# Kernel tuning notes

Measured on AMD Instinct MI355X. Metric: run time of the kernel, lower is better.

## Reference

```python
import jax, jax.numpy as jnp
import numpy as np

N = 100000
E = 1600000
IN_C, HID_C, OUT_C = 128, 128, 64


def setup_inputs() -> dict:
    key = jax.random.key(0)
    ks = jax.random.split(key, 8)
    x = jax.random.normal(ks[0], (N, IN_C), dtype=jnp.float32)
    edge_index = jax.random.randint(ks[1], (2, E), 0, N, dtype=jnp.int64)
    # Glorot-ish init for the 3 GCNConv linear weights + zero biases (PyG default)
    def glorot(k, fan_in, fan_out):
        s = jnp.sqrt(6.0 / (fan_in + fan_out))
        return jax.random.uniform(k, (fan_in, fan_out), jnp.float32, -s, s)
    return {
        "x": x,
        "edge_index": edge_index,
        "W1": glorot(ks[2], IN_C, HID_C), "b1": jnp.zeros((HID_C,), jnp.float32),
        "W2": glorot(ks[3], HID_C, HID_C), "b2": jnp.zeros((HID_C,), jnp.float32),
        "W3": glorot(ks[4], HID_C, OUT_C), "b3": jnp.zeros((OUT_C,), jnp.float32),
    }


def _gcn_norm(edge_index, num_nodes):
    # add self loops, compute D^-1/2 (A+I) D^-1/2 edge coefficients (PyG gcn_norm)
    loop = jnp.arange(num_nodes, dtype=edge_index.dtype)
    src = jnp.concatenate([edge_index[0], loop])  # [E+N]
    dst = jnp.concatenate([edge_index[1], loop])
    w = jnp.ones_like(src, dtype=jnp.float32)
    deg = jax.ops.segment_sum(w, dst, num_segments=num_nodes)
    dinv = jnp.where(deg > 0, jax.lax.rsqrt(deg), 0.0)
    norm = dinv[src] * dinv[dst]  # [E+N]
    return src, dst, norm


def _gcn_layer(x, src, dst, norm, W, b, num_nodes):
    h = x @ W                                   # [N, out]
    msg = h[src] * norm[:, None]                # gather + scale, [E+N, out]
    agg = jax.ops.segment_sum(msg, dst, num_segments=num_nodes)  # scatter-add
    return agg + b


def reference(x, edge_index, W1, b1, W2, b2, W3, b3):
    src, dst, norm = _gcn_norm(edge_index, N)
    h = jax.nn.relu(_gcn_layer(x, src, dst, norm, W1, b1, N))
    h = jax.nn.relu(_gcn_layer(h, src, dst, norm, W2, b2, N))
    h = _gcn_layer(h, src, dst, norm, W3, b3, N)
    return jax.nn.log_softmax(h, axis=-1)  # [N, OUT_C]
```

## Files before the change

kernel.cpp:

```cpp
#include <hip/hip_runtime.h>
#include <hip/hip_bf16.h>


constexpr int N_NODES = 100000;
constexpr int E_EDGES = 1600000;
constexpr int NB = (N_NODES + 127) / 128;
constexpr int BCAP = 2560;
constexpr int CHUNK = 4096;
constexpr int NCHUNK = (E_EDGES + CHUNK - 1) / CHUNK;

typedef short bf16x8 __attribute__((ext_vector_type(8)));
typedef float f32x4 __attribute__((ext_vector_type(4)));

__device__ __forceinline__ unsigned short f2bf(float f) {
    unsigned u = __float_as_uint(f);
    unsigned r = (u + 0x7fff + ((u >> 16) & 1)) >> 16;
    return (unsigned short)r;
}
__device__ __forceinline__ float bf_lo(unsigned u) { return __uint_as_float(u << 16); }
__device__ __forceinline__ float bf_hi(unsigned u) { return __uint_as_float(u & 0xffff0000u); }
__device__ __forceinline__ unsigned pack2bf(float lo, float hi) {
    return (unsigned)f2bf(lo) | ((unsigned)f2bf(hi) << 16);
}

__device__ __forceinline__ int get_idx(const void* ei, int use64, long long pos) {
    if (use64) return (int)((const long long*)ei)[pos];
    return ((const int*)ei)[pos];
}

__global__ void prep_wt_kernel(const float* __restrict__ W1, const float* __restrict__ W2,
                               const float* __restrict__ W3,
                               unsigned short* __restrict__ WT1,
                               unsigned short* __restrict__ WT2,
                               unsigned short* __restrict__ WT3,
                               const int* __restrict__ ei32, int* __restrict__ flag,
                               int* __restrict__ cursorPad) {
    const int b = blockIdx.x;
    if (b == 3) {
        for (int i = threadIdx.x; i < NB * 16; i += blockDim.x) cursorPad[i] = 0;
        if (threadIdx.x == 0) {
            int ok64 = 1;
#pragma unroll
            for (int i = 1; i < 64; i += 2) ok64 &= (ei32[i] == 0);
            *flag = ok64;
        }
        return;
    }
    const float* W = (b == 0) ? W1 : (b == 1) ? W2 : W3;
    unsigned short* WT = (b == 0) ? WT1 : (b == 1) ? WT2 : WT3;
    const int COUT = (b == 2) ? 64 : 128;
    for (int i = threadIdx.x; i < COUT * 128; i += blockDim.x) {
        int c = i >> 7;
        int k = i & 127;
        WT[c * 128 + k] = f2bf(W[k * COUT + c]);
    }
}

__global__ __launch_bounds__(256) void scatter_direct(
    const void* __restrict__ ei, const int* __restrict__ flag,
    int* __restrict__ cursorPad, unsigned* __restrict__ pairs) {
    __shared__ int h[NB];
    __shared__ int base[NB];
    __shared__ unsigned dstb[CHUNK];
    const int t = threadIdx.x;
    const int use64 = *flag;
    const int e0 = blockIdx.x * CHUNK;
    const int e1 = min(E_EDGES, e0 + CHUNK);

    for (int i = t; i < NB; i += 256) h[i] = 0;
    __syncthreads();
    for (int e = e0 + t; e < e1; e += 256) {
        unsigned d = (unsigned)get_idx(ei, use64, (long long)E_EDGES + e);
        dstb[e - e0] = d;
        atomicAdd(&h[d >> 7], 1);
    }
    __syncthreads();
    for (int i = t; i < NB; i += 256) {
        int c = h[i];
        if (c) base[i] = atomicAdd(&cursorPad[i * 16], c);
        h[i] = 0;
    }
    __syncthreads();
    for (int e = e0 + t; e < e1; e += 256) {
        unsigned s = (unsigned)get_idx(ei, use64, e);
        unsigned d = dstb[e - e0];
        int b = d >> 7;
        int r = base[b] + atomicAdd(&h[b], 1);
        if (r < BCAP) pairs[(unsigned)b * BCAP + r] = (s << 7) | (d & 127u);
    }
}

__global__ __launch_bounds__(256) void fine_sort_kernel(
    const unsigned* __restrict__ pairs, const int* __restrict__ cursorPad,
    int* __restrict__ csr, int* __restrict__ rowptr, int* __restrict__ deg,
    float* __restrict__ dinv) {
    __shared__ int h[128];
    __shared__ int rp[128];
    __shared__ int sc[128];
    const int t = threadIdx.x;
    const int b = blockIdx.x;
    const int base = b * BCAP;
    const int cnt = min(cursorPad[b * 16], BCAP);

    if (t < 128) h[t] = 0;
    __syncthreads();
    for (int i = t; i < cnt; i += 256) {
        unsigned p = pairs[base + i];
        atomicAdd(&h[p & 127u], 1);
    }
    __syncthreads();
    int v = (t < 128) ? h[t] : 0;
    if (t < 128) sc[t] = v;
    __syncthreads();
    int incl = v;
    for (int off = 1; off < 128; off <<= 1) {
        int add = (t >= off && t < 128) ? sc[t - off] : 0;
        __syncthreads();
        if (t < 128) {
            incl += add;
            sc[t] = incl;
        }
        __syncthreads();
    }
    if (t < 128) {
        rp[t] = incl - v;
        int node = b * 128 + t;
        if (node < N_NODES) {
            rowptr[node] = base + incl - v;
            deg[node] = v;
            dinv[node] = rsqrtf((float)(v + 1));
        }
        h[t] = 0;
    }
    __syncthreads();
    for (int i = t; i < cnt; i += 256) {
        unsigned p = pairs[base + i];
        int l = (int)(p & 127u);
        int r = atomicAdd(&h[l], 1);
        csr[base + rp[l] + r] = (int)(p >> 7);
    }
}

template <int COUT>
__global__ __launch_bounds__(256) void gemm_mfma_f32(const float* __restrict__ X,
                                                     const unsigned short* __restrict__ WT,
                                                     const float* __restrict__ dinv,
                                                     unsigned short* __restrict__ H) {
    constexpr int NT = COUT / 16;
    __shared__ short Albs[64 * 128];
    __shared__ short Wlds[COUT * 128];

    const int t = threadIdx.x;
    const int row0 = blockIdx.x * 64;

    for (int i = t; i < COUT * 16; i += 256) {
        int n = i >> 4, k8 = i & 15;
        bf16x8 v = *(const bf16x8*)&WT[n * 128 + k8 * 8];
        int ns = (n & ~15) | ((n & 15) ^ k8);
        *(bf16x8*)&Wlds[(k8 * COUT + ns) * 8] = v;
    }
    for (int i = t; i < 1024; i += 256) {
        int m = i >> 4, k8 = i & 15;
        int gr = min(row0 + m, N_NODES - 1);
        const float* p = &X[(size_t)gr * 128 + k8 * 8];
        float4 f0 = *(const float4*)p;
        float4 f1 = *(const float4*)(p + 4);
        bf16x8 v;
        v[0] = (short)f2bf(f0.x); v[1] = (short)f2bf(f0.y);
        v[2] = (short)f2bf(f0.z); v[3] = (short)f2bf(f0.w);
        v[4] = (short)f2bf(f1.x); v[5] = (short)f2bf(f1.y);
        v[6] = (short)f2bf(f1.z); v[7] = (short)f2bf(f1.w);
        int u = ((m >> 4) * 16 + k8) * 16 + ((m & 15) ^ k8);
        *(bf16x8*)&Albs[u * 8] = v;
    }
    __syncthreads();

    const int lane = t & 63;
    const int wv = t >> 6;
    const int l15 = lane & 15;
    const int quad = lane >> 4;

    f32x4 acc[NT];
#pragma unroll
    for (int ct = 0; ct < NT; ct++) acc[ct] = (f32x4){0.f, 0.f, 0.f, 0.f};

#pragma unroll
    for (int kcg = 0; kcg < 4; kcg++) {
        const int k8 = kcg * 4 + quad;
        bf16x8 a = *(const bf16x8*)&Albs[((wv * 16 + k8) * 16 + (l15 ^ k8)) * 8];
#pragma unroll
        for (int ct = 0; ct < NT; ct++) {
            bf16x8 b = *(const bf16x8*)&Wlds[(k8 * COUT + ct * 16 + (l15 ^ k8)) * 8];
            acc[ct] = __builtin_amdgcn_mfma_f32_16x16x32_bf16(a, b, acc[ct], 0, 0, 0);
        }
    }

    const int m0 = row0 + wv * 16;
#pragma unroll
    for (int r = 0; r < 4; r++) {
        int m = m0 + quad * 4 + r;
        if (m < N_NODES) {
            float dv = dinv[m];
#pragma unroll
            for (int ct = 0; ct < NT; ct++)
                H[(size_t)m * COUT + ct * 16 + l15] = f2bf(acc[ct][r] * dv);
        } else if (m == N_NODES) {
#pragma unroll
            for (int ct = 0; ct < NT; ct++)
                H[(size_t)m * COUT + ct * 16 + l15] = 0;
        }
    }
}

template <int COUT>
__global__ __launch_bounds__(256) void gemm_mfma_bf16(const unsigned short* __restrict__ X,
                                                      const unsigned short* __restrict__ WT,
                                                      const float* __restrict__ dinv,
                                                      unsigned short* __restrict__ H) {
    constexpr int NT = COUT / 16;
    __shared__ short Albs[64 * 128];
    __shared__ short Wlds[COUT * 128];

    const int t = threadIdx.x;
    const int row0 = blockIdx.x * 64;

    for (int i = t; i < COUT * 16; i += 256) {
        int n = i >> 4, k8 = i & 15;
        bf16x8 v = *(const bf16x8*)&WT[n * 128 + k8 * 8];
        int ns = (n & ~15) | ((n & 15) ^ k8);
        *(bf16x8*)&Wlds[(k8 * COUT + ns) * 8] = v;
    }
    for (int i = t; i < 1024; i += 256) {
        int m = i >> 4, k8 = i & 15;
        int gr = min(row0 + m, N_NODES - 1);
        bf16x8 v = *(const bf16x8*)&X[(size_t)gr * 128 + k8 * 8];
        int u = ((m >> 4) * 16 + k8) * 16 + ((m & 15) ^ k8);
        *(bf16x8*)&Albs[u * 8] = v;
    }
    __syncthreads();

    const int lane = t & 63;
    const int wv = t >> 6;
    const int l15 = lane & 15;
    const int quad = lane >> 4;

    f32x4 acc[NT];
#pragma unroll
    for (int ct = 0; ct < NT; ct++) acc[ct] = (f32x4){0.f, 0.f, 0.f, 0.f};

#pragma unroll
    for (int kcg = 0; kcg < 4; kcg++) {
        const int k8 = kcg * 4 + quad;
        bf16x8 a = *(const bf16x8*)&Albs[((wv * 16 + k8) * 16 + (l15 ^ k8)) * 8];
#pragma unroll
        for (int ct = 0; ct < NT; ct++) {
            bf16x8 b = *(const bf16x8*)&Wlds[(k8 * COUT + ct * 16 + (l15 ^ k8)) * 8];
            acc[ct] = __builtin_amdgcn_mfma_f32_16x16x32_bf16(a, b, acc[ct], 0, 0, 0);
        }
    }

    const int m0 = row0 + wv * 16;
#pragma unroll
    for (int r = 0; r < 4; r++) {
        int m = m0 + quad * 4 + r;
        if (m < N_NODES) {
            float dv = dinv[m];
#pragma unroll
            for (int ct = 0; ct < NT; ct++)
                H[(size_t)m * COUT + ct * 16 + l15] = f2bf(acc[ct][r] * dv);
        } else if (m == N_NODES) {
#pragma unroll
            for (int ct = 0; ct < NT; ct++)
                H[(size_t)m * COUT + ct * 16 + l15] = 0;
        }
    }
}

__global__ __launch_bounds__(256) void aggregate128_pair(
    const unsigned short* __restrict__ Hb, const int* __restrict__ rowptr,
    const int* __restrict__ deg, const int* __restrict__ csr,
    const float* __restrict__ dinv, const float* __restrict__ bias,
    unsigned short* __restrict__ out) {
    const int lane = threadIdx.x & 63;
    const int wv = threadIdx.x >> 6;
    const int li = lane & 31;
    const int half = lane >> 5;
    const int n = blockIdx.x * 8 + wv * 2 + half;
    const unsigned li8 = (unsigned)li * 8u;
    const char* Hc = (const char*)Hb;

    uint2 s = *(const uint2*)(Hc + (size_t)n * 256u + li8);
    float a0 = bf_lo(s.x), a1 = bf_hi(s.x), a2 = bf_lo(s.y), a3 = bf_hi(s.y);

    const int start = rowptr[n];
    const int dc = deg[n];
    const int dmax = max(dc, __shfl_xor(dc, 32));

    for (int eb = 0; eb < dmax; eb += 32) {
        int myidx = N_NODES;
        if (eb + li < dc) myidx = csr[start + eb + li];
        const int jmax = min(32, dmax - eb);
        int j = 0;
        for (; j + 16 <= jmax; j += 16) {
            int idx[16];
            uint2 u[16];
#pragma unroll
            for (int q = 0; q < 16; q++) idx[q] = __shfl(myidx, j + q, 32);
#pragma unroll
            for (int q = 0; q < 16; q++)
                u[q] = *(const uint2*)(Hc + (((unsigned)idx[q] << 8) + li8));
#pragma unroll
            for (int q = 0; q < 16; q++) {
                a0 += bf_lo(u[q].x); a1 += bf_hi(u[q].x);
                a2 += bf_lo(u[q].y); a3 += bf_hi(u[q].y);
            }
        }
        for (; j + 8 <= jmax; j += 8) {
            int idx[8];
            uint2 u[8];
#pragma unroll
            for (int q = 0; q < 8; q++) idx[q] = __shfl(myidx, j + q, 32);
#pragma unroll
            for (int q = 0; q < 8; q++)
                u[q] = *(const uint2*)(Hc + (((unsigned)idx[q] << 8) + li8));
#pragma unroll
            for (int q = 0; q < 8; q++) {
                a0 += bf_lo(u[q].x); a1 += bf_hi(u[q].x);
                a2 += bf_lo(u[q].y); a3 += bf_hi(u[q].y);
            }
        }
        for (; j + 4 <= jmax; j += 4) {
            int idx[4];
            uint2 u[4];
#pragma unroll
            for (int q = 0; q < 4; q++) idx[q] = __shfl(myidx, j + q, 32);
#pragma unroll
            for (int q = 0; q < 4; q++)
                u[q] = *(const uint2*)(Hc + (((unsigned)idx[q] << 8) + li8));
#pragma unroll
            for (int q = 0; q < 4; q++) {
                a0 += bf_lo(u[q].x); a1 += bf_hi(u[q].x);
                a2 += bf_lo(u[q].y); a3 += bf_hi(u[q].y);
            }
        }
        for (; j < jmax; j++) {
            int i0 = __shfl(myidx, j, 32);
            uint2 u0 = *(const uint2*)(Hc + (((unsigned)i0 << 8) + li8));
            a0 += bf_lo(u0.x); a1 += bf_hi(u0.x);
            a2 += bf_lo(u0.y); a3 += bf_hi(u0.y);
        }
    }

    const float dn = dinv[n];
    float4 bv = *(const float4*)((const char*)bias + li * 16);
    uint2 o;
    o.x = pack2bf(fmaxf(a0 * dn + bv.x, 0.f), fmaxf(a1 * dn + bv.y, 0.f));
    o.y = pack2bf(fmaxf(a2 * dn + bv.z, 0.f), fmaxf(a3 * dn + bv.w, 0.f));
    *(uint2*)((char*)out + (size_t)n * 256 + li * 8) = o;
}

__global__ __launch_bounds__(256) void aggregate64_lsm_pair(
    const unsigned short* __restrict__ Hb, const int* __restrict__ rowptr,
    const int* __restrict__ deg, const int* __restrict__ csr,
    const float* __restrict__ dinv, const float* __restrict__ bias,
    float* __restrict__ out) {
    const int lane = threadIdx.x & 63;
    const int wv = threadIdx.x >> 6;
    const int li = lane & 31;
    const int half = lane >> 5;
    const int n = blockIdx.x * 8 + wv * 2 + half;
    const unsigned li4 = (unsigned)li * 4u;
    const char* Hc = (const char*)Hb;

    unsigned s = *(const unsigned*)(Hc + (size_t)n * 128u + li4);
    float a0 = bf_lo(s), a1 = bf_hi(s);

    const int start = rowptr[n];
    const int dc = deg[n];
    const int dmax = max(dc, __shfl_xor(dc, 32));

    for (int eb = 0; eb < dmax; eb += 32) {
        int myidx = N_NODES;
        if (eb + li < dc) myidx = csr[start + eb + li];
        const int jmax = min(32, dmax - eb);
        int j = 0;
        for (; j + 16 <= jmax; j += 16) {
            int idx[16];
            unsigned u[16];
#pragma unroll
            for (int q = 0; q < 16; q++) idx[q] = __shfl(myidx, j + q, 32);
#pragma unroll
            for (int q = 0; q < 16; q++)
                u[q] = *(const unsigned*)(Hc + (((unsigned)idx[q] << 7) + li4));
#pragma unroll
            for (int q = 0; q < 16; q++) { a0 += bf_lo(u[q]); a1 += bf_hi(u[q]); }
        }
        for (; j + 8 <= jmax; j += 8) {
            int idx[8];
            unsigned u[8];
#pragma unroll
            for (int q = 0; q < 8; q++) idx[q] = __shfl(myidx, j + q, 32);
#pragma unroll
            for (int q = 0; q < 8; q++)
                u[q] = *(const unsigned*)(Hc + (((unsigned)idx[q] << 7) + li4));
#pragma unroll
            for (int q = 0; q < 8; q++) { a0 += bf_lo(u[q]); a1 += bf_hi(u[q]); }
        }
        for (; j + 4 <= jmax; j += 4) {
            int idx[4];
            unsigned u[4];
#pragma unroll
            for (int q = 0; q < 4; q++) idx[q] = __shfl(myidx, j + q, 32);
#pragma unroll
            for (int q = 0; q < 4; q++)
                u[q] = *(const unsigned*)(Hc + (((unsigned)idx[q] << 7) + li4));
#pragma unroll
            for (int q = 0; q < 4; q++) { a0 += bf_lo(u[q]); a1 += bf_hi(u[q]); }
        }
        for (; j < jmax; j++) {
            int i0 = __shfl(myidx, j, 32);
            unsigned u0 = *(const unsigned*)(Hc + (((unsigned)i0 << 7) + li4));
            a0 += bf_lo(u0); a1 += bf_hi(u0);
        }
    }

    const float dn = dinv[n];
    float2 bv = *(const float2*)((const char*)bias + li * 8);
    float v0 = a0 * dn + bv.x;
    float v1 = a1 * dn + bv.y;

    float m = fmaxf(v0, v1);
#pragma unroll
    for (int off = 16; off; off >>= 1) m = fmaxf(m, __shfl_xor(m, off));
    float e = expf(v0 - m) + expf(v1 - m);
#pragma unroll
    for (int off = 16; off; off >>= 1) e += __shfl_xor(e, off);
    float lse = m + logf(e);
    float2 o = make_float2(v0 - lse, v1 - lse);
    *(float2*)((char*)out + (size_t)n * 256 + li * 8) = o;
}

extern "C" void kernel_launch(void* const* d_in, const int* in_sizes, int n_in,
                              void* d_out, int out_size, void* d_ws, size_t ws_size,
                              hipStream_t stream) {
    const float* x = (const float*)d_in[0];
    const void* ei = d_in[1];
    const float* W1 = (const float*)d_in[2];
    const float* b1 = (const float*)d_in[3];
    const float* W2 = (const float*)d_in[4];
    const float* b2 = (const float*)d_in[5];
    const float* W3 = (const float*)d_in[6];
    const float* b3 = (const float*)d_in[7];
    float* out = (float*)d_out;

    char* w = (char*)d_ws;
    size_t off = 0;
    auto take = [&](size_t bytes) {
        char* p = w + off;
        off = (off + bytes + 255) & ~(size_t)255;
        return p;
    };
    int* flag = (int*)take(4);
    int* cursorPad = (int*)take((size_t)NB * 64);
    int* deg = (int*)take((size_t)N_NODES * 4);
    int* rowptr = (int*)take((size_t)N_NODES * 4);
    float* dinv = (float*)take((size_t)N_NODES * 4);
    int* csr = (int*)take((size_t)NB * BCAP * 4);
    unsigned short* WT1 = (unsigned short*)take(128 * 128 * 2);
    unsigned short* WT2 = (unsigned short*)take(128 * 128 * 2);
    unsigned short* WT3 = (unsigned short*)take(64 * 128 * 2);
    unsigned short* A = (unsigned short*)take((size_t)(N_NODES + 1) * 128 * 2);
    unsigned short* B = (unsigned short*)take((size_t)N_NODES * 128 * 2);
    unsigned* pairs = (unsigned*)A;

    prep_wt_kernel<<<4, 256, 0, stream>>>(W1, W2, W3, WT1, WT2, WT3,
                                          (const int*)ei, flag, cursorPad);
    scatter_direct<<<NCHUNK, 256, 0, stream>>>(ei, flag, cursorPad, pairs);
    fine_sort_kernel<<<NB, 256, 0, stream>>>(pairs, cursorPad, csr, rowptr, deg, dinv);

    const int gg = (N_NODES + 63) / 64;
    const int gagg = N_NODES / 8;

    gemm_mfma_f32<128><<<gg, 256, 0, stream>>>(x, WT1, dinv, A);
    aggregate128_pair<<<gagg, 256, 0, stream>>>(A, rowptr, deg, csr, dinv, b1, B);
    gemm_mfma_bf16<128><<<gg, 256, 0, stream>>>(B, WT2, dinv, A);
    aggregate128_pair<<<gagg, 256, 0, stream>>>(A, rowptr, deg, csr, dinv, b2, B);
    gemm_mfma_bf16<64><<<gg, 256, 0, stream>>>(B, WT3, dinv, A);
    aggregate64_lsm_pair<<<gagg, 256, 0, stream>>>(A, rowptr, deg, csr, dinv, b3, out);
}
```

Before: 361.9 us.

## Fuse aggregation with the next layer's GEMM via an LDS tile

Each 8-node aggregation block now writes its ReLU'd bf16 rows into a shared-memory tile (padded to 16 rows with zeros) and immediately multiplies them by the next layer's weight matrix with MFMA, writing the scaled next-layer H directly. This removes the two standalone bf16 GEMM kernels and the global round trip of the intermediate activations. In exchange, every block reloads the full weight matrix into LDS (up to 32KB per block), which lowers occupancy for the latency-bound gather. Half of each MFMA tile is wasted padding. Ping-pong buffers are swapped, and B is enlarged to hold the zero sentinel row.

```diff
diff --git a/kernel.cpp b/kernel.cpp
--- a/kernel.cpp
+++ b/kernel.cpp
@@ -213,76 +213,31 @@
 }
 
 template <int COUT>
-__global__ __launch_bounds__(256) void gemm_mfma_bf16(const unsigned short* __restrict__ X,
-                                                      const unsigned short* __restrict__ WT,
-                                                      const float* __restrict__ dinv,
-                                                      unsigned short* __restrict__ H) {
-    constexpr int NT = COUT / 16;
-    __shared__ short Albs[64 * 128];
-    __shared__ short Wlds[COUT * 128];
-
-    const int t = threadIdx.x;
-    const int row0 = blockIdx.x * 64;
-
-    for (int i = t; i < COUT * 16; i += 256) {
-        int n = i >> 4, k8 = i & 15;
-        bf16x8 v = *(const bf16x8*)&WT[n * 128 + k8 * 8];
-        int ns = (n & ~15) | ((n & 15) ^ k8);
-        *(bf16x8*)&Wlds[(k8 * COUT + ns) * 8] = v;
-    }
-    for (int i = t; i < 1024; i += 256) {
-        int m = i >> 4, k8 = i & 15;
-        int gr = min(row0 + m, N_NODES - 1);
-        bf16x8 v = *(const bf16x8*)&X[(size_t)gr * 128 + k8 * 8];
-        int u = ((m >> 4) * 16 + k8) * 16 + ((m & 15) ^ k8);
-        *(bf16x8*)&Albs[u * 8] = v;
-    }
-    __syncthreads();
-
-    const int lane = t & 63;
-    const int wv = t >> 6;
-    const int l15 = lane & 15;
-    const int quad = lane >> 4;
-
-    f32x4 acc[NT];
-#pragma unroll
-    for (int ct = 0; ct < NT; ct++) acc[ct] = (f32x4){0.f, 0.f, 0.f, 0.f};
-
-#pragma unroll
-    for (int kcg = 0; kcg < 4; kcg++) {
-        const int k8 = kcg * 4 + quad;
-        bf16x8 a = *(const bf16x8*)&Albs[((wv * 16 + k8) * 16 + (l15 ^ k8)) * 8];
-#pragma unroll
-        for (int ct = 0; ct < NT; ct++) {
-            bf16x8 b = *(const bf16x8*)&Wlds[(k8 * COUT + ct * 16 + (l15 ^ k8)) * 8];
-            acc[ct] = __builtin_amdgcn_mfma_f32_16x16x32_bf16(a, b, acc[ct], 0, 0, 0);
-        }
-    }
-
-    const int m0 = row0 + wv * 16;
-#pragma unroll
-    for (int r = 0; r < 4; r++) {
-        int m = m0 + quad * 4 + r;
-        if (m < N_NODES) {
-            float dv = dinv[m];
-#pragma unroll
-            for (int ct = 0; ct < NT; ct++)
-                H[(size_t)m * COUT + ct * 16 + l15] = f2bf(acc[ct][r] * dv);
-        } else if (m == N_NODES) {
-#pragma unroll
-            for (int ct = 0; ct < NT; ct++)
-                H[(size_t)m * COUT + ct * 16 + l15] = 0;
-        }
-    }
-}
-
-__global__ __launch_bounds__(256) void aggregate128_pair(
+__global__ __launch_bounds__(256) void agg128_fused(
     const unsigned short* __restrict__ Hb, const int* __restrict__ rowptr,
     const int* __restrict__ deg, const int* __restrict__ csr,
     const float* __restrict__ dinv, const float* __restrict__ bias,
-    unsigned short* __restrict__ out) {
-    const int lane = threadIdx.x & 63;
-    const int wv = threadIdx.x >> 6;
+    const unsigned short* __restrict__ WT, unsigned short* __restrict__ Hn) {
+    constexpr int NT = COUT / 16;
+    constexpr int CTW = NT / 4;
+    __shared__ short Wlds[COUT * 128];
+    __shared__ short Atile[16 * 128];
+
+    const int t = threadIdx.x;
+
+    for (int i = t; i < COUT * 16; i += 256) {
+        int nn = i >> 4, k8 = i & 15;
+        bf16x8 v = *(const bf16x8*)&WT[nn * 128 + k8 * 8];
+        int ns = (nn & ~15) | ((nn & 15) ^ k8);
+        *(bf16x8*)&Wlds[(k8 * COUT + ns) * 8] = v;
+    }
+    if (t < 128) {
+        int k8z = t >> 3, mm = 8 + (t & 7);
+        *(uint4*)&Atile[(k8z * 16 + (mm ^ k8z)) * 8] = (uint4){0u, 0u, 0u, 0u};
+    }
+
+    const int lane = t & 63;
+    const int wv = t >> 6;
     const int li = lane & 31;
     const int half = lane >> 5;
     const int n = blockIdx.x * 8 + wv * 2 + half;
@@ -351,12 +306,52 @@
         }
     }
 
-    const float dn = dinv[n];
-    float4 bv = *(const float4*)((const char*)bias + li * 16);
-    uint2 o;
-    o.x = pack2bf(fmaxf(a0 * dn + bv.x, 0.f), fmaxf(a1 * dn + bv.y, 0.f));
-    o.y = pack2bf(fmaxf(a2 * dn + bv.z, 0.f), fmaxf(a3 * dn + bv.w, 0.f));
-    *(uint2*)((char*)out + (size_t)n * 256 + li * 8) = o;
+    {
+        const float dn = dinv[n];
+        float4 bv = *(const float4*)((const char*)bias + li * 16);
+        unsigned w0 = pack2bf(fmaxf(a0 * dn + bv.x, 0.f), fmaxf(a1 * dn + bv.y, 0.f));
+        unsigned w1 = pack2bf(fmaxf(a2 * dn + bv.z, 0.f), fmaxf(a3 * dn + bv.w, 0.f));
+        const int r = wv * 2 + half;
+        const int k8 = li >> 1;
+        uint2 o; o.x = w0; o.y = w1;
+        *(uint2*)&Atile[(k8 * 16 + (r ^ k8)) * 8 + (li & 1) * 4] = o;
+    }
+    __syncthreads();
+
+    const int l15 = lane & 15;
+    const int quad = lane >> 4;
+    f32x4 acc[CTW];
+#pragma unroll
+    for (int c = 0; c < CTW; c++) acc[c] = (f32x4){0.f, 0.f, 0.f, 0.f};
+
+#pragma unroll
+    for (int kcg = 0; kcg < 4; kcg++) {
+        const int k8 = kcg * 4 + quad;
+        bf16x8 a = *(const bf16x8*)&Atile[(k8 * 16 + (l15 ^ k8)) * 8];
+#pragma unroll
+        for (int c = 0; c < CTW; c++) {
+            const int ct = wv * CTW + c;
+            bf16x8 b = *(const bf16x8*)&Wlds[(k8 * COUT + ct * 16 + (l15 ^ k8)) * 8];
+            acc[c] = __builtin_amdgcn_mfma_f32_16x16x32_bf16(a, b, acc[c], 0, 0, 0);
+        }
+    }
+
+#pragma unroll
+    for (int rr = 0; rr < 4; rr++) {
+        const int row = quad * 4 + rr;
+        if (row < 8) {
+            const int m = blockIdx.x * 8 + row;
+            const float dv = dinv[m];
+#pragma unroll
+            for (int c = 0; c < CTW; c++) {
+                const int ct = wv * CTW + c;
+                Hn[(size_t)m * COUT + ct * 16 + l15] = f2bf(acc[c][rr] * dv);
+            }
+        }
+    }
+
+    if (blockIdx.x == 0 && t < COUT / 4)
+        *(unsigned long long*)((char*)Hn + (size_t)N_NODES * (COUT * 2) + t * 8) = 0ull;
 }
 
 __global__ __launch_bounds__(256) void aggregate64_lsm_pair(
@@ -470,7 +465,7 @@
     unsigned short* WT2 = (unsigned short*)take(128 * 128 * 2);
     unsigned short* WT3 = (unsigned short*)take(64 * 128 * 2);
     unsigned short* A = (unsigned short*)take((size_t)(N_NODES + 1) * 128 * 2);
-    unsigned short* B = (unsigned short*)take((size_t)N_NODES * 128 * 2);
+    unsigned short* B = (unsigned short*)take((size_t)(N_NODES + 1) * 128 * 2);
     unsigned* pairs = (unsigned*)A;
 
     prep_wt_kernel<<<4, 256, 0, stream>>>(W1, W2, W3, WT1, WT2, WT3,
@@ -479,12 +474,10 @@
     fine_sort_kernel<<<NB, 256, 0, stream>>>(pairs, cursorPad, csr, rowptr, deg, dinv);
 
     const int gg = (N_NODES + 63) / 64;
-    const int gagg = N_NODES / 8;
+    const int g8 = N_NODES / 8;
 
     gemm_mfma_f32<128><<<gg, 256, 0, stream>>>(x, WT1, dinv, A);
-    aggregate128_pair<<<gagg, 256, 0, stream>>>(A, rowptr, deg, csr, dinv, b1, B);
-    gemm_mfma_bf16<128><<<gg, 256, 0, stream>>>(B, WT2, dinv, A);
-    aggregate128_pair<<<gagg, 256, 0, stream>>>(A, rowptr, deg, csr, dinv, b2, B);
-    gemm_mfma_bf16<64><<<gg, 256, 0, stream>>>(B, WT3, dinv, A);
-    aggregate64_lsm_pair<<<gagg, 256, 0, stream>>>(A, rowptr, deg, csr, dinv, b3, out);
-}
+    agg128_fused<128><<<g8, 256, 0, stream>>>(A, rowptr, deg, csr, dinv, b1, WT2, B);
+    agg128_fused<64><<<g8, 256, 0, stream>>>(B, rowptr, deg, csr, dinv, b2, WT3, A);
+    aggregate64_lsm_pair<<<g8, 256, 0, stream>>>(A, rowptr, deg, csr, dinv, b3, out);
+}
```

Result: slower. 378.7 us (+4.6%).

## Locally bucket-sort edges in LDS before writing scatter pairs to global

Applied to the files above, without the earlier changes.

The scatter kernel now reads src and dst in a single pass and computes per-bucket local offsets with a block-wide prefix scan. It then packs edges contiguously by bucket in shared memory and writes each bucket's run to global memory. The aim is to cut random global writes and the second pass over the edge index. In exchange it uses more shared memory, adds a scan with many barriers, and ends with a serial per-thread copy loop whose load is uneven across lanes.

```diff
diff --git a/kernel.cpp b/kernel.cpp
--- a/kernel.cpp
+++ b/kernel.cpp
@@ -60,33 +60,90 @@
     const void* __restrict__ ei, const int* __restrict__ flag,
     int* __restrict__ cursorPad, unsigned* __restrict__ pairs) {
     __shared__ int h[NB];
-    __shared__ int base[NB];
-    __shared__ unsigned dstb[CHUNK];
+    __shared__ int lofs[NB];
+    __shared__ int gbase[NB];
+    __shared__ int scanbuf[256];
+    __shared__ unsigned ebuf[CHUNK];
+    __shared__ unsigned short ebkt[CHUNK];
+    __shared__ unsigned pairbuf[CHUNK];
+
     const int t = threadIdx.x;
     const int use64 = *flag;
     const int e0 = blockIdx.x * CHUNK;
     const int e1 = min(E_EDGES, e0 + CHUNK);
+    const int n = e1 - e0;
 
     for (int i = t; i < NB; i += 256) h[i] = 0;
     __syncthreads();
-    for (int e = e0 + t; e < e1; e += 256) {
-        unsigned d = (unsigned)get_idx(ei, use64, (long long)E_EDGES + e);
-        dstb[e - e0] = d;
-        atomicAdd(&h[d >> 7], 1);
-    }
-    __syncthreads();
-    for (int i = t; i < NB; i += 256) {
-        int c = h[i];
-        if (c) base[i] = atomicAdd(&cursorPad[i * 16], c);
-        h[i] = 0;
-    }
-    __syncthreads();
-    for (int e = e0 + t; e < e1; e += 256) {
-        unsigned s = (unsigned)get_idx(ei, use64, e);
-        unsigned d = dstb[e - e0];
-        int b = d >> 7;
-        int r = base[b] + atomicAdd(&h[b], 1);
-        if (r < BCAP) pairs[(unsigned)b * BCAP + r] = (s << 7) | (d & 127u);
+
+    for (int k = 0; k < CHUNK / 256; k++) {
+        const int i = k * 256 + t;
+        const int e = e0 + i;
+        if (e < e1) {
+            unsigned s = (unsigned)get_idx(ei, use64, e);
+            unsigned d = (unsigned)get_idx(ei, use64, (long long)E_EDGES + e);
+            ebuf[i] = (s << 7) | (d & 127u);
+            unsigned b = d >> 7;
+            ebkt[i] = (unsigned short)b;
+            atomicAdd(&h[b], 1);
+        } else {
+            ebkt[i] = 0xFFFFu;
+        }
+    }
+    __syncthreads();
+
+    {
+        const int B0 = t * 4;
+        int c0 = 0, c1 = 0, c2 = 0, c3 = 0, s0 = 0;
+        if (B0 + 0 < NB) { c0 = h[B0 + 0]; s0 += c0; }
+        if (B0 + 1 < NB) { c1 = h[B0 + 1]; s0 += c1; }
+        if (B0 + 2 < NB) { c2 = h[B0 + 2]; s0 += c2; }
+        if (B0 + 3 < NB) { c3 = h[B0 + 3]; s0 += c3; }
+        scanbuf[t] = s0;
+        __syncthreads();
+        int incl = s0;
+        for (int off = 1; off < 256; off <<= 1) {
+            int add = (t >= off) ? scanbuf[t - off] : 0;
+            __syncthreads();
+            incl += add;
+            scanbuf[t] = incl;
+            __syncthreads();
+        }
+        int run = incl - s0;
+        int cc[4] = {c0, c1, c2, c3};
+#pragma unroll
+        for (int q = 0; q < 4; q++) {
+            int b = B0 + q;
+            if (b < NB) {
+                lofs[b] = run;
+                if (cc[q]) gbase[b] = atomicAdd(&cursorPad[b * 16], cc[q]);
+                h[b] = 0;
+                run += cc[q];
+            }
+        }
+    }
+    __syncthreads();
+
+    for (int k = 0; k < CHUNK / 256; k++) {
+        const int i = k * 256 + t;
+        const unsigned b = ebkt[i];
+        if (b != 0xFFFFu) {
+            int r = atomicAdd(&h[b], 1);
+            pairbuf[lofs[b] + r] = ebuf[i];
+        }
+    }
+    __syncthreads();
+
+    for (int b = t; b < NB; b += 256) {
+        const int c = h[b];
+        if (!c) continue;
+        const int lo = lofs[b];
+        const int gb = gbase[b];
+        unsigned* dst = &pairs[(unsigned)b * BCAP];
+        for (int r = 0; r < c; r++) {
+            const int idx = gb + r;
+            if (idx < BCAP) dst[idx] = pairbuf[lo + r];
+        }
     }
 }
 
```

Result: no change. 360.5 us (-0.4%).

## Replace bucketed pair sort with global-atomic degree count and direct CSR scatter

Applied to the files above, without the earlier changes.

The two-pass block-bucketed CSR build (LDS histogram, coarse scatter of packed pairs, then a fine per-bucket sort) is replaced by three simple kernels. They count per-node degree with global atomics, build row pointers with a per-128-node block scan into fixed-capacity buckets, and scatter source ids into CSR slots using a per-node global atomic cursor. The zeroing of the degree and cursor arrays is spread across extra blocks of the prep kernel. This drops the intermediate pairs buffer and the LDS work, but it relies on many more contended global atomics and on random scattered writes.

```diff
diff --git a/kernel.cpp b/kernel.cpp
--- a/kernel.cpp
+++ b/kernel.cpp
@@ -6,8 +6,7 @@
 constexpr int E_EDGES = 1600000;
 constexpr int NB = (N_NODES + 127) / 128;
 constexpr int BCAP = 2560;
-constexpr int CHUNK = 4096;
-constexpr int NCHUNK = (E_EDGES + CHUNK - 1) / CHUNK;
+constexpr int DEGN = 100032;
 
 typedef short bf16x8 __attribute__((ext_vector_type(8)));
 typedef float f32x4 __attribute__((ext_vector_type(4)));
@@ -34,11 +33,16 @@
                                unsigned short* __restrict__ WT2,
                                unsigned short* __restrict__ WT3,
                                const int* __restrict__ ei32, int* __restrict__ flag,
-                               int* __restrict__ cursorPad) {
+                               int* __restrict__ degcur) {
     const int b = blockIdx.x;
-    if (b == 3) {
-        for (int i = threadIdx.x; i < NB * 16; i += blockDim.x) cursorPad[i] = 0;
-        if (threadIdx.x == 0) {
+    if (b >= 3) {
+        const int total = 2 * DEGN;
+        const int per = (total + 8) / 9;
+        const int z = b - 3;
+        const int lo = z * per;
+        const int hi = min(total, lo + per);
+        for (int i = lo + threadIdx.x; i < hi; i += blockDim.x) degcur[i] = 0;
+        if (b == 3 && threadIdx.x == 0) {
             int ok64 = 1;
 #pragma unroll
             for (int i = 1; i < 64; i += 2) ok64 &= (ei32[i] == 0);
@@ -56,89 +60,49 @@
     }
 }
 
-__global__ __launch_bounds__(256) void scatter_direct(
+__global__ __launch_bounds__(256) void deg_count_kernel(
     const void* __restrict__ ei, const int* __restrict__ flag,
-    int* __restrict__ cursorPad, unsigned* __restrict__ pairs) {
-    __shared__ int h[NB];
-    __shared__ int base[NB];
-    __shared__ unsigned dstb[CHUNK];
-    const int t = threadIdx.x;
+    int* __restrict__ deg) {
+    const int e = blockIdx.x * 256 + threadIdx.x;
     const int use64 = *flag;
-    const int e0 = blockIdx.x * CHUNK;
-    const int e1 = min(E_EDGES, e0 + CHUNK);
-
-    for (int i = t; i < NB; i += 256) h[i] = 0;
-    __syncthreads();
-    for (int e = e0 + t; e < e1; e += 256) {
-        unsigned d = (unsigned)get_idx(ei, use64, (long long)E_EDGES + e);
-        dstb[e - e0] = d;
-        atomicAdd(&h[d >> 7], 1);
-    }
-    __syncthreads();
-    for (int i = t; i < NB; i += 256) {
-        int c = h[i];
-        if (c) base[i] = atomicAdd(&cursorPad[i * 16], c);
-        h[i] = 0;
-    }
-    __syncthreads();
-    for (int e = e0 + t; e < e1; e += 256) {
-        unsigned s = (unsigned)get_idx(ei, use64, e);
-        unsigned d = dstb[e - e0];
-        int b = d >> 7;
-        int r = base[b] + atomicAdd(&h[b], 1);
-        if (r < BCAP) pairs[(unsigned)b * BCAP + r] = (s << 7) | (d & 127u);
-    }
-}
-
-__global__ __launch_bounds__(256) void fine_sort_kernel(
-    const unsigned* __restrict__ pairs, const int* __restrict__ cursorPad,
-    int* __restrict__ csr, int* __restrict__ rowptr, int* __restrict__ deg,
+    unsigned d = (unsigned)get_idx(ei, use64, (long long)E_EDGES + e);
+    atomicAdd(&deg[d], 1);
+}
+
+__global__ __launch_bounds__(128) void rowptr_kernel(
+    const int* __restrict__ deg, int* __restrict__ rowptr,
     float* __restrict__ dinv) {
-    __shared__ int h[128];
-    __shared__ int rp[128];
     __shared__ int sc[128];
     const int t = threadIdx.x;
-    const int b = blockIdx.x;
-    const int base = b * BCAP;
-    const int cnt = min(cursorPad[b * 16], BCAP);
-
-    if (t < 128) h[t] = 0;
-    __syncthreads();
-    for (int i = t; i < cnt; i += 256) {
-        unsigned p = pairs[base + i];
-        atomicAdd(&h[p & 127u], 1);
-    }
-    __syncthreads();
-    int v = (t < 128) ? h[t] : 0;
-    if (t < 128) sc[t] = v;
+    const int node = blockIdx.x * 128 + t;
+    int v = (node < N_NODES) ? deg[node] : 0;
+    sc[t] = v;
     __syncthreads();
     int incl = v;
     for (int off = 1; off < 128; off <<= 1) {
-        int add = (t >= off && t < 128) ? sc[t - off] : 0;
+        int add = (t >= off) ? sc[t - off] : 0;
         __syncthreads();
-        if (t < 128) {
-            incl += add;
-            sc[t] = incl;
-        }
+        incl += add;
+        sc[t] = incl;
         __syncthreads();
     }
-    if (t < 128) {
-        rp[t] = incl - v;
-        int node = b * 128 + t;
-        if (node < N_NODES) {
-            rowptr[node] = base + incl - v;
-            deg[node] = v;
-            dinv[node] = rsqrtf((float)(v + 1));
-        }
-        h[t] = 0;
-    }
-    __syncthreads();
-    for (int i = t; i < cnt; i += 256) {
-        unsigned p = pairs[base + i];
-        int l = (int)(p & 127u);
-        int r = atomicAdd(&h[l], 1);
-        csr[base + rp[l] + r] = (int)(p >> 7);
-    }
+    if (node < N_NODES) {
+        rowptr[node] = blockIdx.x * BCAP + incl - v;
+        dinv[node] = rsqrtf((float)(v + 1));
+    }
+}
+
+__global__ __launch_bounds__(256) void edge_scatter_kernel(
+    const void* __restrict__ ei, const int* __restrict__ flag,
+    const int* __restrict__ rowptr, int* __restrict__ cur,
+    int* __restrict__ csr) {
+    const int e = blockIdx.x * 256 + threadIdx.x;
+    const int use64 = *flag;
+    int s = get_idx(ei, use64, e);
+    unsigned d = (unsigned)get_idx(ei, use64, (long long)E_EDGES + e);
+    int r = atomicAdd(&cur[d], 1);
+    int pos = rowptr[d] + r;
+    if (pos < (int)(((d >> 7) + 1) * BCAP)) csr[pos] = s;
 }
 
 template <int COUT>
@@ -461,8 +425,9 @@
         return p;
     };
     int* flag = (int*)take(4);
-    int* cursorPad = (int*)take((size_t)NB * 64);
-    int* deg = (int*)take((size_t)N_NODES * 4);
+    int* degcur = (int*)take((size_t)2 * DEGN * 4);
+    int* deg = degcur;
+    int* cur = degcur + DEGN;
     int* rowptr = (int*)take((size_t)N_NODES * 4);
     float* dinv = (float*)take((size_t)N_NODES * 4);
     int* csr = (int*)take((size_t)NB * BCAP * 4);
@@ -471,12 +436,12 @@
     unsigned short* WT3 = (unsigned short*)take(64 * 128 * 2);
     unsigned short* A = (unsigned short*)take((size_t)(N_NODES + 1) * 128 * 2);
     unsigned short* B = (unsigned short*)take((size_t)N_NODES * 128 * 2);
-    unsigned* pairs = (unsigned*)A;
-
-    prep_wt_kernel<<<4, 256, 0, stream>>>(W1, W2, W3, WT1, WT2, WT3,
-                                          (const int*)ei, flag, cursorPad);
-    scatter_direct<<<NCHUNK, 256, 0, stream>>>(ei, flag, cursorPad, pairs);
-    fine_sort_kernel<<<NB, 256, 0, stream>>>(pairs, cursorPad, csr, rowptr, deg, dinv);
+
+    prep_wt_kernel<<<12, 256, 0, stream>>>(W1, W2, W3, WT1, WT2, WT3,
+                                           (const int*)ei, flag, degcur);
+    deg_count_kernel<<<E_EDGES / 256, 256, 0, stream>>>(ei, flag, deg);
+    rowptr_kernel<<<NB, 128, 0, stream>>>(deg, rowptr, dinv);
+    edge_scatter_kernel<<<E_EDGES / 256, 256, 0, stream>>>(ei, flag, rowptr, cur, csr);
 
     const int gg = (N_NODES + 63) / 64;
     const int gagg = N_NODES / 8;
```

Result: slower. 482.4 us (+33.3%).
